# Kernel tuning notes

Measured on AMD Instinct MI355X. Metric: run time of the kernel, lower is better.

## Reference

```python
import jax, jax.numpy as jnp
import numpy as np

EMBED_DIM = 2048
NUM_HEADS = 16
HEAD_DIM = EMBED_DIM // NUM_HEADS
ROPE_BASE = 10000.0


def setup_inputs() -> dict:
    key = jax.random.key(0)
    ks = jax.random.split(key, 5)
    s = 1.0 / np.sqrt(EMBED_DIM)
    return {
        "x": jax.random.normal(ks[0], (2, 2048, EMBED_DIM), dtype=jnp.float32),
        "Wq": jax.random.normal(ks[1], (EMBED_DIM, EMBED_DIM), dtype=jnp.float32) * s,
        "Wk": jax.random.normal(ks[2], (EMBED_DIM, EMBED_DIM), dtype=jnp.float32) * s,
        "Wv": jax.random.normal(ks[3], (EMBED_DIM, EMBED_DIM), dtype=jnp.float32) * s,
        "Wo": jax.random.normal(ks[4], (EMBED_DIM, EMBED_DIM), dtype=jnp.float32) * s,
    }


def _rope(x):
    # x: [b, h, s, d]; standard rotate-half RoPE
    b, h, s, d = x.shape
    inv_freq = 1.0 / (ROPE_BASE ** (jnp.arange(0, d, 2, dtype=jnp.float32) / d))
    ang = jnp.arange(s, dtype=jnp.float32)[:, None] * inv_freq[None, :]  # [s, d/2]
    cos = jnp.concatenate([jnp.cos(ang), jnp.cos(ang)], axis=-1)  # [s, d]
    sin = jnp.concatenate([jnp.sin(ang), jnp.sin(ang)], axis=-1)
    x1, x2 = x[..., : d // 2], x[..., d // 2 :]
    rot = jnp.concatenate([-x2, x1], axis=-1)
    return x * cos + rot * sin


def reference(x, Wq, Wk, Wv, Wo):
    b, s, e = x.shape
    h, d = NUM_HEADS, HEAD_DIM
    # projections (torch Linear: x @ W.T); W here stored so that y = x @ W
    q = (x @ Wq).reshape(b, s, h, d).transpose(0, 2, 1, 3)
    k = (x @ Wk).reshape(b, s, h, d).transpose(0, 2, 1, 3)
    v = (x @ Wv).reshape(b, s, h, d).transpose(0, 2, 1, 3)
    q = _rope(q)
    k = _rope(k)
    att = jnp.einsum("bhqd,bhkd->bhqk", q, k) / jnp.sqrt(jnp.float32(d))
    causal = jnp.tril(jnp.ones((s, s), dtype=bool))
    att = jnp.where(causal, att, -jnp.inf)
    att = jax.nn.softmax(att, axis=-1)
    out = jnp.einsum("bhqk,bhkd->bhqd", att, v)
    out = out.transpose(0, 2, 1, 3).reshape(b, s, e)
    return out @ Wo
```

## Files before the change

kernel.cpp:

```cpp
#include <hip/hip_runtime.h>
#include <stdint.h>

#define EDIM 2048
#define HH 16
#define DD 128
#define SS 2048
#define BB 2
#define NT2 32

typedef __attribute__((ext_vector_type(8))) __bf16 bf16x8;
typedef __attribute__((ext_vector_type(8))) unsigned short ushort8;
typedef __attribute__((ext_vector_type(4))) unsigned short ushort4v;
typedef __attribute__((ext_vector_type(4))) float f32x4;

#define MFMA16 __builtin_amdgcn_mfma_f32_16x16x32_bf16

__device__ __forceinline__ unsigned short f2b(float f) {
    union { float f; unsigned int u; } v; v.f = f;
    unsigned int u = v.u;
    unsigned int r = (u + 0x7fffu + ((u >> 16) & 1u)) >> 16;
    return (unsigned short)r;
}
__device__ __forceinline__ float b2f(unsigned short h) {
    union { unsigned int u; float f; } v; v.u = ((unsigned int)h) << 16;
    return v.f;
}
__device__ __forceinline__ bf16x8 lds8(const unsigned short* p) {
    return __builtin_bit_cast(bf16x8, *(const ushort8*)p);
}
__device__ __forceinline__ void gl_lds16(const unsigned short* g, unsigned short* l) {
    __builtin_amdgcn_global_load_lds(
        (const __attribute__((address_space(1))) void*)(const void*)g,
        (__attribute__((address_space(3))) void*)(void*)l, 16, 0, 0);
}
__device__ __forceinline__ float fexp2(float x) {
    float r;
    asm volatile("v_exp_f32 %0, %1\n\ts_nop 1" : "=v"(r) : "v"(x));
    return r;
}
__device__ __forceinline__ void barrier_np() {
    __builtin_amdgcn_s_barrier();
    __builtin_amdgcn_sched_barrier(0);
}


__global__ __launch_bounds__(256) void k_cvt_x(const float4* __restrict__ x,
                                               ushort4v* __restrict__ xb) {
    size_t i = (size_t)blockIdx.x * 256 + threadIdx.x;
    float4 v = x[i];
    ushort4v o;
    o.x = f2b(v.x); o.y = f2b(v.y); o.z = f2b(v.z); o.w = f2b(v.w);
    xb[i] = o;
}

__global__ __launch_bounds__(256) void k_trans(const float* __restrict__ W0,
                                               const float* __restrict__ W1,
                                               const float* __restrict__ W2,
                                               const float* __restrict__ W3,
                                               unsigned short* __restrict__ Wt) {
    const float* W = (blockIdx.z == 0) ? W0 : (blockIdx.z == 1) ? W1
                     : (blockIdx.z == 2) ? W2 : W3;
    unsigned short* out = Wt + (size_t)blockIdx.z * EDIM * EDIM;
    __shared__ float t[64][65];
    int r0 = blockIdx.y * 64, c0 = blockIdx.x * 64;
#pragma unroll
    for (int i = 0; i < 16; ++i) {
        int e = threadIdx.x + i * 256; int r = e >> 6, c = e & 63;
        t[r][c] = W[(size_t)(r0 + r) * EDIM + c0 + c];
    }
    __syncthreads();
#pragma unroll
    for (int i = 0; i < 16; ++i) {
        int e = threadIdx.x + i * 256; int r = e >> 6, c = e & 63;
        out[(size_t)(c0 + r) * EDIM + r0 + c] = f2b(t[c][r]);
    }
}


__device__ __forceinline__ void stage16(const unsigned short* __restrict__ G,
                                        unsigned short* L, int wave, int lane, int s) {
    int q  = (s * 8 + wave) * 1024 + lane * 16;
    int qp = q ^ (((q >> 7) & 7) << 4);
    int row = qp >> 7, col = (qp & 127) >> 1;
    gl_lds16(G + (size_t)row * EDIM + col, L + (s * 8 + wave) * 512);
}
__device__ __forceinline__ bf16x8 frag_read(const unsigned short* Lhalf,
                                            int rowl, int kk, int lg) {
    int b = rowl * 128 + kk * 64 + lg * 16;
    b ^= ((b >> 7) & 7) << 4;
    return lds8(Lhalf + (b >> 1));
}

#define QKV_PHASE(MF0) do {                                                    \
    bf16x8 a00 = frag_read(Ah, (MF0) * 16 + lr, 0, lg);                        \
    bf16x8 a01 = frag_read(Ah, (MF0) * 16 + lr, 1, lg);                        \
    bf16x8 a10 = frag_read(Ah, (MF0) * 16 + 16 + lr, 0, lg);                   \
    bf16x8 a11 = frag_read(Ah, (MF0) * 16 + 16 + lr, 1, lg);                   \
    __builtin_amdgcn_s_setprio(1);                                             \
    _Pragma("unroll")                                                          \
    for (int nf = 0; nf < 4; ++nf) {                                           \
        acc[(MF0)][nf]     = MFMA16(a00, bfr[nf][0], acc[(MF0)][nf], 0, 0, 0); \
        acc[(MF0)][nf]     = MFMA16(a01, bfr[nf][1], acc[(MF0)][nf], 0, 0, 0); \
        acc[(MF0) + 1][nf] = MFMA16(a10, bfr[nf][0], acc[(MF0) + 1][nf], 0, 0, 0); \
        acc[(MF0) + 1][nf] = MFMA16(a11, bfr[nf][1], acc[(MF0) + 1][nf], 0, 0, 0); \
    }                                                                          \
    __builtin_amdgcn_s_setprio(0);                                             \
} while (0)

__global__ __launch_bounds__(512) void k_gemm_qkv2(const unsigned short* __restrict__ xb,
                                                   const unsigned short* __restrict__ Wt,
                                                   unsigned short* __restrict__ Qd,
                                                   unsigned short* __restrict__ Kd,
                                                   unsigned short* __restrict__ Vtd) {
    __shared__ alignas(16) unsigned short As[2][2][8192];
    __shared__ alignas(16) unsigned short Bs[2][2][8192];
    const int tid = threadIdx.x, wave = tid >> 6, lane = tid & 63;
    const int lr = lane & 15, lg = lane >> 4;
    const int wm = wave >> 2, wn = wave & 3;
    const int nb   = (blockIdx.x & 7) * 48 + (blockIdx.x >> 3);
    const int wsel = nb >> 7, rr = nb & 127;
    const size_t m0 = (size_t)(rr & 15) * 256;
    const size_t n0 = (size_t)(rr >> 4) * 256;
    const unsigned short* A  = xb;
    const unsigned short* Bw = Wt + (size_t)wsel * EDIM * EDIM;

    f32x4 acc[8][4] = {};

#pragma unroll
    for (int h = 0; h < 2; ++h)
#pragma unroll
        for (int s = 0; s < 2; ++s)
            stage16(Bw + (n0 + h * 128) * EDIM, Bs[0][h], wave, lane, s);
#pragma unroll
    for (int h = 0; h < 2; ++h)
#pragma unroll
        for (int s = 0; s < 2; ++s)
            stage16(A + (m0 + h * 128) * EDIM, As[0][h], wave, lane, s);
#pragma unroll
    for (int h = 0; h < 2; ++h)
#pragma unroll
        for (int s = 0; s < 2; ++s)
            stage16(Bw + (n0 + h * 128) * EDIM + 64, Bs[1][h], wave, lane, s);
    asm volatile("s_waitcnt vmcnt(4)" ::: "memory");
    __builtin_amdgcn_sched_barrier(0);
    barrier_np();

    for (int u = 0; u < NT2; ++u) {
        const int cur = u & 1;
        const unsigned short* Ah = As[cur][wm];
        bf16x8 bfr[4][2];
#pragma unroll
        for (int nf = 0; nf < 4; ++nf) {
            int nl = wn * 64 + nf * 16 + lr;
            const unsigned short* Bh = Bs[cur][nl >> 7];
#pragma unroll
            for (int kk = 0; kk < 2; ++kk)
                bfr[nf][kk] = frag_read(Bh, nl & 127, kk, lg);
        }
        QKV_PHASE(0);
        barrier_np();
        if (u + 1 < NT2) {
#pragma unroll
            for (int h = 0; h < 2; ++h)
#pragma unroll
                for (int s = 0; s < 2; ++s)
                    stage16(A + (m0 + h * 128) * EDIM + (u + 1) * 64,
                            As[(u + 1) & 1][h], wave, lane, s);
        }
        QKV_PHASE(2);
        barrier_np();
        if (u + 2 < NT2) {
#pragma unroll
            for (int h = 0; h < 2; ++h)
#pragma unroll
                for (int s = 0; s < 2; ++s)
                    stage16(Bw + (n0 + h * 128) * EDIM + (u + 2) * 64,
                            Bs[cur][h], wave, lane, s);
        }
        QKV_PHASE(4);
        barrier_np();
        QKV_PHASE(6);
        if (u + 2 < NT2) asm volatile("s_waitcnt vmcnt(4)" ::: "memory");
        else             asm volatile("s_waitcnt vmcnt(0)" ::: "memory");
        __builtin_amdgcn_sched_barrier(0);
        barrier_np();
    }

    if (wsel < 2) {
        unsigned short* dst = wsel ? Kd : Qd;
#pragma unroll
        for (int mf = 0; mf < 8; ++mf)
#pragma unroll
            for (int nf = 0; nf < 4; ++nf)
#pragma unroll
                for (int r = 0; r < 4; ++r) {
                    int row = (int)m0 + wm * 128 + mf * 16 + lg * 4 + r;
                    int e   = (int)n0 + wn * 64 + nf * 16 + lr;
                    int b = row >> 11, s = row & (SS - 1);
                    int h = e >> 7,  d = e & (DD - 1);
                    dst[(((size_t)(b * HH + h)) * SS + s) * DD + d] = f2b(acc[mf][nf][r]);
                }
    } else {
#pragma unroll
        for (int mf = 0; mf < 8; ++mf)
#pragma unroll
            for (int nf = 0; nf < 4; ++nf) {
                int row0 = (int)m0 + wm * 128 + mf * 16 + lg * 4;
                int e    = (int)n0 + wn * 64 + nf * 16 + lr;
                int b = row0 >> 11, s0 = row0 & (SS - 1);
                int h = e >> 7, d = e & (DD - 1);
                ushort4v pk;
                pk.x = f2b(acc[mf][nf][0]); pk.y = f2b(acc[mf][nf][1]);
                pk.z = f2b(acc[mf][nf][2]); pk.w = f2b(acc[mf][nf][3]);
                *(ushort4v*)(Vtd + (((size_t)(b * HH + h)) * DD + d) * SS + s0) = pk;
            }
    }
}


__device__ __forceinline__ void gemm_core(const unsigned short* __restrict__ A,
                                          const unsigned short* __restrict__ Bt,
                                          int K, size_t m0, size_t n0,
                                          unsigned short* As, unsigned short* Bs,
                                          f32x4 acc[4][4], int wave, int lane) {
    const int wm = wave >> 1, wn = wave & 1;
    const int lg = lane >> 4, lr = lane & 15;
    for (int kt = 0; kt < K; kt += 32) {
#pragma unroll
        for (int j = 0; j < 2; ++j) {
            const int cb = j * 256 + wave * 64;
            const int c  = cb + lane;
            gl_lds16(A  + (m0 + (size_t)(c >> 2)) * K + kt + (c & 3) * 8, As + cb * 8);
            gl_lds16(Bt + (n0 + (size_t)(c >> 2)) * K + kt + (c & 3) * 8, Bs + cb * 8);
        }
        __syncthreads();
        bf16x8 af[4], bg[4];
#pragma unroll
        for (int i = 0; i < 4; ++i) {
            af[i] = lds8(As + (wm * 64 + i * 16 + lr) * 32 + lg * 8);
            bg[i] = lds8(Bs + (wn * 64 + i * 16 + lr) * 32 + lg * 8);
        }
#pragma unroll
        for (int i = 0; i < 4; ++i)
#pragma unroll
            for (int j = 0; j < 4; ++j)
                acc[i][j] = MFMA16(af[i], bg[j], acc[i][j], 0, 0, 0);
        __syncthreads();
    }
}

__global__ __launch_bounds__(256) void k_gemm_out(const unsigned short* __restrict__ Ob,
                                                  const unsigned short* __restrict__ Wto,
                                                  float* __restrict__ y) {
    __shared__ alignas(16) unsigned short As[128 * 32];
    __shared__ alignas(16) unsigned short Bs[128 * 32];
    const int tid = threadIdx.x, wave = tid >> 6, lane = tid & 63;
    const int nb = (blockIdx.x & 7) * 64 + (blockIdx.x >> 3);
    const size_t m0 = (size_t)(nb & 31) * 128;
    const size_t n0 = (size_t)(nb >> 5) * 128;
    f32x4 acc[4][4] = {};
    gemm_core(Ob, Wto, EDIM, m0, n0, As, Bs, acc, wave, lane);
    const int wm = wave >> 1, wn = wave & 1, lg = lane >> 4, lr = lane & 15;
#pragma unroll
    for (int i = 0; i < 4; ++i)
#pragma unroll
        for (int j = 0; j < 4; ++j)
#pragma unroll
            for (int r = 0; r < 4; ++r) {
                size_t row = m0 + wm * 64 + i * 16 + lg * 4 + r;
                size_t col = n0 + wn * 64 + j * 16 + lr;
                y[row * EDIM + col] = acc[i][j][r];
            }
}


__global__ __launch_bounds__(256) void k_rope(unsigned short* __restrict__ Q,
                                              unsigned short* __restrict__ K) {
    int idx = blockIdx.x * 256 + threadIdx.x;
    int i  = idx & 63;
    int s  = (idx >> 6) & (SS - 1);
    int bh = idx >> 17;
    size_t base = ((size_t)bh * SS + s) * DD;
    float inv = __expf(-0.14391156608f * (float)i);
    float ang = (float)s * inv;
    float sn, cs; sincosf(ang, &sn, &cs);
    const float qs = 0.08838834764831845f * 1.44269504088896340736f;
    float q1 = b2f(Q[base + i]), q2 = b2f(Q[base + 64 + i]);
    float k1 = b2f(K[base + i]), k2 = b2f(K[base + 64 + i]);
    Q[base + i]      = f2b((q1 * cs - q2 * sn) * qs);
    Q[base + 64 + i] = f2b((q2 * cs + q1 * sn) * qs);
    K[base + i]      = f2b(k1 * cs - k2 * sn);
    K[base + 64 + i] = f2b(k2 * cs + k1 * sn);
}


__device__ __forceinline__ void attn_tile(const unsigned short* Ks, const unsigned short* Vs,
                                          unsigned short* Ps, const bf16x8 qf[4],
                                          f32x4 o[9], bool maskdiag,
                                          int wave, int lg, int lr) {
    f32x4 sa[4] = {};
    __builtin_amdgcn_s_setprio(1);
#pragma unroll
    for (int nf = 0; nf < 4; ++nf)
#pragma unroll
        for (int kk = 0; kk < 4; ++kk) {
            bf16x8 kb = lds8(Ks + (nf * 16 + lr) * 136 + kk * 32 + lg * 8);
            sa[nf] = MFMA16(qf[kk], kb, sa[nf], 0, 0, 0);
        }
    __builtin_amdgcn_s_setprio(0);
    if (maskdiag) {
#pragma unroll
        for (int nf = 0; nf < 4; ++nf)
#pragma unroll
            for (int r = 0; r < 4; ++r) {
                int col = nf * 16 + lr, rw = wave * 16 + lg * 4 + r;
                if (col > rw) sa[nf][r] = -__builtin_inff();
            }
    }
#pragma unroll
    for (int nf = 0; nf < 4; ++nf)
#pragma unroll
        for (int r = 0; r < 4; ++r) {
            float p = fexp2(sa[nf][r]);
            unsigned int u = __builtin_bit_cast(unsigned int, p);
            Ps[(wave * 16 + lg * 4 + r) * 72 + nf * 16 + lr] =
                (unsigned short)((u + 0x8000u) >> 16);
        }
    bf16x8 pa0 = lds8(Ps + (wave * 16 + lr) * 72 + lg * 8);
    bf16x8 pa1 = lds8(Ps + (wave * 16 + lr) * 72 + 32 + lg * 8);
    __builtin_amdgcn_s_setprio(1);
#pragma unroll
    for (int nf = 0; nf < 9; ++nf) {
        bf16x8 v0 = lds8(Vs + (nf * 16 + lr) * 72 + lg * 8);
        bf16x8 v1 = lds8(Vs + (nf * 16 + lr) * 72 + 32 + lg * 8);
        o[nf] = MFMA16(pa0, v0, o[nf], 0, 0, 0);
        o[nf] = MFMA16(pa1, v1, o[nf], 0, 0, 0);
    }
    __builtin_amdgcn_s_setprio(0);
}

__global__ __launch_bounds__(256) void k_attn(const unsigned short* __restrict__ Q,
                                              const unsigned short* __restrict__ Kg,
                                              const unsigned short* __restrict__ Vt,
                                              unsigned short* __restrict__ Ob) {
    __shared__ alignas(16) unsigned short Ks[64 * 136];
    __shared__ alignas(16) unsigned short Vs[144 * 72];
    __shared__ alignas(16) unsigned short Ps[64 * 72];
    const int tid = threadIdx.x, wave = tid >> 6, lane = tid & 63;
    const int lg = lane >> 4, lr = lane & 15;
    const int bh = blockIdx.y;
    const int tp = blockIdx.x;
    const int qa0 = tp * 64, qb0 = (31 - tp) * 64;
    const int nta = tp + 1, ntb = 32 - tp;
    const size_t qkb = (size_t)bh * SS * DD;
    const size_t vbb = (size_t)bh * DD * SS;
    {
        ushort4v one4; one4.x = 0x3F80; one4.y = 0x3F80; one4.z = 0x3F80; one4.w = 0x3F80;
        *(ushort4v*)(Vs + (128 + (tid >> 4)) * 72 + (tid & 15) * 4) = one4;
    }
    bf16x8 qfA[4], qfB[4];
    {
        const unsigned short* qpA = Q + qkb + (size_t)(qa0 + wave * 16 + lr) * DD + lg * 8;
        const unsigned short* qpB = Q + qkb + (size_t)(qb0 + wave * 16 + lr) * DD + lg * 8;
#pragma unroll
        for (int kk = 0; kk < 4; ++kk) {
            qfA[kk] = __builtin_bit_cast(bf16x8, *(const ushort8*)(qpA + kk * 32));
            qfB[kk] = __builtin_bit_cast(bf16x8, *(const ushort8*)(qpB + kk * 32));
        }
    }
    f32x4 oA[9] = {}, oB[9] = {};
    ushort8 kr[4], vr[4];
#pragma unroll
    for (int i = 0; i < 4; ++i) {
        int c = tid + i * 256;
        kr[i] = *(const ushort8*)(Kg + qkb + (size_t)(c >> 4) * DD + (c & 15) * 8);
        vr[i] = *(const ushort8*)(Vt + vbb + (size_t)(c >> 3) * SS + (c & 7) * 8);
    }
    for (int t = 0; t < ntb; ++t) {
        __syncthreads();
#pragma unroll
        for (int i = 0; i < 4; ++i) {
            int c = tid + i * 256;
            *(ushort8*)(Ks + (c >> 4) * 136 + (c & 15) * 8) = kr[i];
            *(ushort8*)(Vs + (c >> 3) * 72 + (c & 7) * 8) = vr[i];
        }
        __syncthreads();
        if (t + 1 < ntb) {
            int kv0 = (t + 1) * 64;
#pragma unroll
            for (int i = 0; i < 4; ++i) {
                int c = tid + i * 256;
                kr[i] = *(const ushort8*)(Kg + qkb + (size_t)(kv0 + (c >> 4)) * DD + (c & 15) * 8);
                vr[i] = *(const ushort8*)(Vt + vbb + (size_t)(c >> 3) * SS + kv0 + (c & 7) * 8);
            }
        }
        attn_tile(Ks, Vs, Ps, qfB, oB, t == ntb - 1, wave, lg, lr);
        if (t < nta)
            attn_tile(Ks, Vs, Ps, qfA, oA, t == nta - 1, wave, lg, lr);
    }
    const int b = bh >> 4, h = bh & 15;
#pragma unroll
    for (int nf = 0; nf < 8; ++nf)
#pragma unroll
        for (int r = 0; r < 4; ++r) {
            int sA = qa0 + wave * 16 + lg * 4 + r;
            int sB = qb0 + wave * 16 + lg * 4 + r;
            int e = h * DD + nf * 16 + lr;
            Ob[((size_t)b * SS + sA) * EDIM + e] = f2b(oA[nf][r] / oA[8][r]);
            Ob[((size_t)b * SS + sB) * EDIM + e] = f2b(oB[nf][r] / oB[8][r]);
        }
}


extern "C" void kernel_launch(void* const* d_in, const int* in_sizes, int n_in,
                              void* d_out, int out_size, void* d_ws, size_t ws_size,
                              hipStream_t stream) {
    const float* x  = (const float*)d_in[0];
    const float* Wq = (const float*)d_in[1];
    const float* Wk = (const float*)d_in[2];
    const float* Wv = (const float*)d_in[3];
    const float* Wo = (const float*)d_in[4];
    float* y = (float*)d_out;
    char* ws = (char*)d_ws;
    unsigned short* xb  = (unsigned short*)(ws);
    unsigned short* Wt  = (unsigned short*)(ws + (size_t)16777216);
    unsigned short* Qd  = (unsigned short*)(ws + (size_t)50331648);
    unsigned short* Kd  = (unsigned short*)(ws + (size_t)67108864);
    unsigned short* Vtd = (unsigned short*)(ws + (size_t)83886080);
    unsigned short* Ob  = (unsigned short*)(ws + (size_t)100663296);

    hipLaunchKernelGGL(k_cvt_x, dim3(8192), dim3(256), 0, stream, (const float4*)x, (ushort4v*)xb);
    hipLaunchKernelGGL(k_trans, dim3(32, 32, 4), dim3(256), 0, stream, Wq, Wk, Wv, Wo, Wt);
    hipLaunchKernelGGL(k_gemm_qkv2, dim3(384), dim3(512), 0, stream, xb, Wt, Qd, Kd, Vtd);
    hipLaunchKernelGGL(k_rope, dim3(16384), dim3(256), 0, stream, Qd, Kd);
    hipLaunchKernelGGL(k_attn, dim3(16, 32), dim3(256), 0, stream, Qd, Kd, Vtd, Ob);
    hipLaunchKernelGGL(k_gemm_out, dim3(512), dim3(256), 0, stream,
                       Ob, Wt + (size_t)3 * EDIM * EDIM, y);
}
```

Measured before the change: 421.7 us.

## Share pipelined 256x128 GEMM core between QKV and output projections

Replaces the 256x256 QKV tile with a shared 256x128 double-buffered, swizzled, async-staged GEMM routine, which doubles the QKV grid to 768 blocks for better wave balance across CUs. The output projection drops its simple 128x128, K=32, synchronous GEMM and uses the same pipelined routine with 512-thread blocks. The goals are better occupancy and balance for the QKV GEMM and better latency hiding for the output GEMM. The cost is a smaller per-block tile, so arithmetic intensity drops and A-tile traffic in QKV rises.

```diff
diff --git a/kernel.cpp b/kernel.cpp
--- a/kernel.cpp
+++ b/kernel.cpp
@@ -91,21 +91,77 @@
     return lds8(Lhalf + (b >> 1));
 }
 
-#define QKV_PHASE(MF0) do {                                                    \
-    bf16x8 a00 = frag_read(Ah, (MF0) * 16 + lr, 0, lg);                        \
-    bf16x8 a01 = frag_read(Ah, (MF0) * 16 + lr, 1, lg);                        \
-    bf16x8 a10 = frag_read(Ah, (MF0) * 16 + 16 + lr, 0, lg);                   \
-    bf16x8 a11 = frag_read(Ah, (MF0) * 16 + 16 + lr, 1, lg);                   \
-    __builtin_amdgcn_s_setprio(1);                                             \
-    _Pragma("unroll")                                                          \
-    for (int nf = 0; nf < 4; ++nf) {                                           \
-        acc[(MF0)][nf]     = MFMA16(a00, bfr[nf][0], acc[(MF0)][nf], 0, 0, 0); \
-        acc[(MF0)][nf]     = MFMA16(a01, bfr[nf][1], acc[(MF0)][nf], 0, 0, 0); \
-        acc[(MF0) + 1][nf] = MFMA16(a10, bfr[nf][0], acc[(MF0) + 1][nf], 0, 0, 0); \
-        acc[(MF0) + 1][nf] = MFMA16(a11, bfr[nf][1], acc[(MF0) + 1][nf], 0, 0, 0); \
-    }                                                                          \
-    __builtin_amdgcn_s_setprio(0);                                             \
+#define GPH(MF) do {                                                        \
+    bf16x8 a0 = frag_read(Ah, ar0 + (MF) * 16 + lr, 0, lg);                 \
+    bf16x8 a1 = frag_read(Ah, ar0 + (MF) * 16 + lr, 1, lg);                 \
+    __builtin_amdgcn_s_setprio(1);                                          \
+    _Pragma("unroll")                                                       \
+    for (int nf = 0; nf < 4; ++nf) {                                        \
+        acc[(MF)][nf] = MFMA16(a0, bfr[nf][0], acc[(MF)][nf], 0, 0, 0);     \
+        acc[(MF)][nf] = MFMA16(a1, bfr[nf][1], acc[(MF)][nf], 0, 0, 0);     \
+    }                                                                       \
+    __builtin_amdgcn_s_setprio(0);                                          \
 } while (0)
+
+__device__ __forceinline__ void gemm_256x128(const unsigned short* __restrict__ A,
+                                             const unsigned short* __restrict__ Bt,
+                                             size_t m0, size_t n0,
+                                             unsigned short As[2][2][8192],
+                                             unsigned short Bs[2][8192],
+                                             f32x4 acc[4][4], int wave, int lane) {
+    const int lr = lane & 15, lg = lane >> 4;
+    const int wm = wave >> 1;
+    const int ah = wm >> 1, ar0 = (wm & 1) * 64;
+    const int wn = wave & 1;
+
+#pragma unroll
+    for (int s = 0; s < 2; ++s) stage16(Bt + n0 * EDIM, Bs[0], wave, lane, s);
+#pragma unroll
+    for (int h = 0; h < 2; ++h)
+#pragma unroll
+        for (int s = 0; s < 2; ++s)
+            stage16(A + (m0 + h * 128) * EDIM, As[0][h], wave, lane, s);
+#pragma unroll
+    for (int s = 0; s < 2; ++s) stage16(Bt + n0 * EDIM + 64, Bs[1], wave, lane, s);
+    asm volatile("s_waitcnt vmcnt(2)" ::: "memory");
+    __builtin_amdgcn_sched_barrier(0);
+    barrier_np();
+
+    for (int u = 0; u < NT2; ++u) {
+        const int cur = u & 1;
+        const unsigned short* Ah = As[cur][ah];
+        bf16x8 bfr[4][2];
+#pragma unroll
+        for (int nf = 0; nf < 4; ++nf)
+#pragma unroll
+            for (int kk = 0; kk < 2; ++kk)
+                bfr[nf][kk] = frag_read(Bs[cur], wn * 64 + nf * 16 + lr, kk, lg);
+        GPH(0);
+        barrier_np();
+        if (u + 1 < NT2) {
+#pragma unroll
+            for (int h = 0; h < 2; ++h)
+#pragma unroll
+                for (int s = 0; s < 2; ++s)
+                    stage16(A + (m0 + h * 128) * EDIM + (u + 1) * 64,
+                            As[(u + 1) & 1][h], wave, lane, s);
+        }
+        GPH(1);
+        barrier_np();
+        if (u + 2 < NT2) {
+#pragma unroll
+            for (int s = 0; s < 2; ++s)
+                stage16(Bt + n0 * EDIM + (u + 2) * 64, Bs[cur], wave, lane, s);
+        }
+        GPH(2);
+        barrier_np();
+        GPH(3);
+        if (u + 2 < NT2) asm volatile("s_waitcnt vmcnt(2)" ::: "memory");
+        else             asm volatile("s_waitcnt vmcnt(0)" ::: "memory");
+        __builtin_amdgcn_sched_barrier(0);
+        barrier_np();
+    }
+}
 
 __global__ __launch_bounds__(512) void k_gemm_qkv2(const unsigned short* __restrict__ xb,
                                                    const unsigned short* __restrict__ Wt,
@@ -113,88 +169,26 @@
                                                    unsigned short* __restrict__ Kd,
                                                    unsigned short* __restrict__ Vtd) {
     __shared__ alignas(16) unsigned short As[2][2][8192];
-    __shared__ alignas(16) unsigned short Bs[2][2][8192];
+    __shared__ alignas(16) unsigned short Bs[2][8192];
     const int tid = threadIdx.x, wave = tid >> 6, lane = tid & 63;
     const int lr = lane & 15, lg = lane >> 4;
-    const int wm = wave >> 2, wn = wave & 3;
-    const int nb   = (blockIdx.x & 7) * 48 + (blockIdx.x >> 3);
-    const int wsel = nb >> 7, rr = nb & 127;
+    const int wm = wave >> 1, wn = wave & 1;
+    const int nb   = (blockIdx.x & 7) * 96 + (blockIdx.x >> 3);
+    const int wsel = nb >> 8, rr = nb & 255;
     const size_t m0 = (size_t)(rr & 15) * 256;
-    const size_t n0 = (size_t)(rr >> 4) * 256;
-    const unsigned short* A  = xb;
-    const unsigned short* Bw = Wt + (size_t)wsel * EDIM * EDIM;
-
-    f32x4 acc[8][4] = {};
-
-#pragma unroll
-    for (int h = 0; h < 2; ++h)
-#pragma unroll
-        for (int s = 0; s < 2; ++s)
-            stage16(Bw + (n0 + h * 128) * EDIM, Bs[0][h], wave, lane, s);
-#pragma unroll
-    for (int h = 0; h < 2; ++h)
-#pragma unroll
-        for (int s = 0; s < 2; ++s)
-            stage16(A + (m0 + h * 128) * EDIM, As[0][h], wave, lane, s);
-#pragma unroll
-    for (int h = 0; h < 2; ++h)
-#pragma unroll
-        for (int s = 0; s < 2; ++s)
-            stage16(Bw + (n0 + h * 128) * EDIM + 64, Bs[1][h], wave, lane, s);
-    asm volatile("s_waitcnt vmcnt(4)" ::: "memory");
-    __builtin_amdgcn_sched_barrier(0);
-    barrier_np();
-
-    for (int u = 0; u < NT2; ++u) {
-        const int cur = u & 1;
-        const unsigned short* Ah = As[cur][wm];
-        bf16x8 bfr[4][2];
-#pragma unroll
-        for (int nf = 0; nf < 4; ++nf) {
-            int nl = wn * 64 + nf * 16 + lr;
-            const unsigned short* Bh = Bs[cur][nl >> 7];
-#pragma unroll
-            for (int kk = 0; kk < 2; ++kk)
-                bfr[nf][kk] = frag_read(Bh, nl & 127, kk, lg);
-        }
-        QKV_PHASE(0);
-        barrier_np();
-        if (u + 1 < NT2) {
-#pragma unroll
-            for (int h = 0; h < 2; ++h)
-#pragma unroll
-                for (int s = 0; s < 2; ++s)
-                    stage16(A + (m0 + h * 128) * EDIM + (u + 1) * 64,
-                            As[(u + 1) & 1][h], wave, lane, s);
-        }
-        QKV_PHASE(2);
-        barrier_np();
-        if (u + 2 < NT2) {
-#pragma unroll
-            for (int h = 0; h < 2; ++h)
-#pragma unroll
-                for (int s = 0; s < 2; ++s)
-                    stage16(Bw + (n0 + h * 128) * EDIM + (u + 2) * 64,
-                            Bs[cur][h], wave, lane, s);
-        }
-        QKV_PHASE(4);
-        barrier_np();
-        QKV_PHASE(6);
-        if (u + 2 < NT2) asm volatile("s_waitcnt vmcnt(4)" ::: "memory");
-        else             asm volatile("s_waitcnt vmcnt(0)" ::: "memory");
-        __builtin_amdgcn_sched_barrier(0);
-        barrier_np();
-    }
+    const size_t n0 = (size_t)(rr >> 4) * 128;
+    f32x4 acc[4][4] = {};
+    gemm_256x128(xb, Wt + (size_t)wsel * EDIM * EDIM, m0, n0, As, Bs, acc, wave, lane);
 
     if (wsel < 2) {
         unsigned short* dst = wsel ? Kd : Qd;
 #pragma unroll
-        for (int mf = 0; mf < 8; ++mf)
+        for (int mf = 0; mf < 4; ++mf)
 #pragma unroll
             for (int nf = 0; nf < 4; ++nf)
 #pragma unroll
                 for (int r = 0; r < 4; ++r) {
-                    int row = (int)m0 + wm * 128 + mf * 16 + lg * 4 + r;
+                    int row = (int)m0 + wm * 64 + mf * 16 + lg * 4 + r;
                     int e   = (int)n0 + wn * 64 + nf * 16 + lr;
                     int b = row >> 11, s = row & (SS - 1);
                     int h = e >> 7,  d = e & (DD - 1);
@@ -202,10 +196,10 @@
                 }
     } else {
 #pragma unroll
-        for (int mf = 0; mf < 8; ++mf)
+        for (int mf = 0; mf < 4; ++mf)
 #pragma unroll
             for (int nf = 0; nf < 4; ++nf) {
-                int row0 = (int)m0 + wm * 128 + mf * 16 + lg * 4;
+                int row0 = (int)m0 + wm * 64 + mf * 16 + lg * 4;
                 int e    = (int)n0 + wn * 64 + nf * 16 + lr;
                 int b = row0 >> 11, s0 = row0 & (SS - 1);
                 int h = e >> 7, d = e & (DD - 1);
@@ -217,59 +211,28 @@
     }
 }
 
-
-__device__ __forceinline__ void gemm_core(const unsigned short* __restrict__ A,
-                                          const unsigned short* __restrict__ Bt,
-                                          int K, size_t m0, size_t n0,
-                                          unsigned short* As, unsigned short* Bs,
-                                          f32x4 acc[4][4], int wave, int lane) {
-    const int wm = wave >> 1, wn = wave & 1;
-    const int lg = lane >> 4, lr = lane & 15;
-    for (int kt = 0; kt < K; kt += 32) {
-#pragma unroll
-        for (int j = 0; j < 2; ++j) {
-            const int cb = j * 256 + wave * 64;
-            const int c  = cb + lane;
-            gl_lds16(A  + (m0 + (size_t)(c >> 2)) * K + kt + (c & 3) * 8, As + cb * 8);
-            gl_lds16(Bt + (n0 + (size_t)(c >> 2)) * K + kt + (c & 3) * 8, Bs + cb * 8);
-        }
-        __syncthreads();
-        bf16x8 af[4], bg[4];
-#pragma unroll
-        for (int i = 0; i < 4; ++i) {
-            af[i] = lds8(As + (wm * 64 + i * 16 + lr) * 32 + lg * 8);
-            bg[i] = lds8(Bs + (wn * 64 + i * 16 + lr) * 32 + lg * 8);
-        }
-#pragma unroll
-        for (int i = 0; i < 4; ++i)
-#pragma unroll
-            for (int j = 0; j < 4; ++j)
-                acc[i][j] = MFMA16(af[i], bg[j], acc[i][j], 0, 0, 0);
-        __syncthreads();
-    }
-}
-
-__global__ __launch_bounds__(256) void k_gemm_out(const unsigned short* __restrict__ Ob,
+__global__ __launch_bounds__(512) void k_gemm_out(const unsigned short* __restrict__ Ob,
                                                   const unsigned short* __restrict__ Wto,
                                                   float* __restrict__ y) {
-    __shared__ alignas(16) unsigned short As[128 * 32];
-    __shared__ alignas(16) unsigned short Bs[128 * 32];
+    __shared__ alignas(16) unsigned short As[2][2][8192];
+    __shared__ alignas(16) unsigned short Bs[2][8192];
     const int tid = threadIdx.x, wave = tid >> 6, lane = tid & 63;
-    const int nb = (blockIdx.x & 7) * 64 + (blockIdx.x >> 3);
-    const size_t m0 = (size_t)(nb & 31) * 128;
-    const size_t n0 = (size_t)(nb >> 5) * 128;
+    const int lr = lane & 15, lg = lane >> 4;
+    const int wm = wave >> 1, wn = wave & 1;
+    const int nb = (blockIdx.x & 7) * 32 + (blockIdx.x >> 3);
+    const size_t m0 = (size_t)(nb & 15) * 256;
+    const size_t n0 = (size_t)(nb >> 4) * 128;
     f32x4 acc[4][4] = {};
-    gemm_core(Ob, Wto, EDIM, m0, n0, As, Bs, acc, wave, lane);
-    const int wm = wave >> 1, wn = wave & 1, lg = lane >> 4, lr = lane & 15;
-#pragma unroll
-    for (int i = 0; i < 4; ++i)
-#pragma unroll
-        for (int j = 0; j < 4; ++j)
+    gemm_256x128(Ob, Wto, m0, n0, As, Bs, acc, wave, lane);
+#pragma unroll
+    for (int mf = 0; mf < 4; ++mf)
+#pragma unroll
+        for (int nf = 0; nf < 4; ++nf)
 #pragma unroll
             for (int r = 0; r < 4; ++r) {
-                size_t row = m0 + wm * 64 + i * 16 + lg * 4 + r;
-                size_t col = n0 + wn * 64 + j * 16 + lr;
-                y[row * EDIM + col] = acc[i][j][r];
+                size_t row = m0 + wm * 64 + mf * 16 + lg * 4 + r;
+                size_t col = n0 + wn * 64 + nf * 16 + lr;
+                y[row * EDIM + col] = acc[mf][nf][r];
             }
 }
 
@@ -431,9 +394,9 @@
 
     hipLaunchKernelGGL(k_cvt_x, dim3(8192), dim3(256), 0, stream, (const float4*)x, (ushort4v*)xb);
     hipLaunchKernelGGL(k_trans, dim3(32, 32, 4), dim3(256), 0, stream, Wq, Wk, Wv, Wo, Wt);
-    hipLaunchKernelGGL(k_gemm_qkv2, dim3(384), dim3(512), 0, stream, xb, Wt, Qd, Kd, Vtd);
+    hipLaunchKernelGGL(k_gemm_qkv2, dim3(768), dim3(512), 0, stream, xb, Wt, Qd, Kd, Vtd);
     hipLaunchKernelGGL(k_rope, dim3(16384), dim3(256), 0, stream, Qd, Kd);
     hipLaunchKernelGGL(k_attn, dim3(16, 32), dim3(256), 0, stream, Qd, Kd, Vtd, Ob);
-    hipLaunchKernelGGL(k_gemm_out, dim3(512), dim3(256), 0, stream,
+    hipLaunchKernelGGL(k_gemm_out, dim3(256), dim3(512), 0, stream,
                        Ob, Wt + (size_t)3 * EDIM * EDIM, y);
 }
```

Result: no change. 424.4 us (+0.6%).
